# Kernel optimization log

Measured on AMD Instinct MI355X. Metric: run time of the kernel, lower is better.

## Reference

```python
import jax, jax.numpy as jnp
import numpy as np

N_NODES = 100000


def gcn_conv(x, edge_index, W, b):
    """GCNConv: out = D^-1/2 (A + I) D^-1/2 (x W) + b, with added self-loops."""
    n = x.shape[0]
    xw = x @ W  # [N, C]
    loop = jnp.arange(n, dtype=edge_index.dtype)
    src = jnp.concatenate([edge_index[0], loop])  # [E+N]
    dst = jnp.concatenate([edge_index[1], loop])
    deg = jax.ops.segment_sum(jnp.ones_like(dst, dtype=xw.dtype), dst, num_segments=n)
    dinv = jax.lax.rsqrt(jnp.where(deg > 0, deg, 1.0))
    norm = dinv[src] * dinv[dst]  # [E+N]
    msgs = xw[src] * norm[:, None]  # gather + scale
    out = jax.ops.segment_sum(msgs, dst, num_segments=n)  # scatter-add
    return out + b


def setup_inputs() -> dict:
    key = jax.random.key(0)
    k1, k2, k3, k4, k5 = jax.random.split(key, 5)
    F_in, C1, C2 = 256, 64, 40
    E = 3200000
    x = jax.random.normal(k1, (N_NODES, F_in), dtype=jnp.float32)
    edge_index = jax.random.randint(k2, (2, E), 0, N_NODES, dtype=jnp.int64)
    W1 = jax.random.normal(k3, (F_in, C1), dtype=jnp.float32) / np.sqrt(F_in)
    b1 = jnp.zeros((C1,), dtype=jnp.float32)
    W2 = jax.random.normal(k4, (C1, C2), dtype=jnp.float32) / np.sqrt(C1)
    b2 = jnp.zeros((C2,), dtype=jnp.float32)
    return {"x": x, "edge_index": edge_index, "W1": W1, "b1": b1, "W2": W2, "b2": b2}


def reference(x, edge_index, W1, b1, W2, b2):
    h1 = jax.nn.relu(gcn_conv(x, edge_index, W1, b1))
    # dropout is identity in eval mode (training=False)
    h2 = gcn_conv(h1, edge_index, W2, b2)
    return jax.nn.log_softmax(h2, axis=1)
```

## Files before the change

### kernel.cpp

```cpp
#include <hip/hip_runtime.h>
#include <math.h>

#define NN 100000
#define NB 256
#define RANGE 392
#define CAP 56
#define BCAP 13824
#define NBLK_PART 512

typedef unsigned int uint;
typedef __attribute__((ext_vector_type(8))) short short8;
typedef __attribute__((ext_vector_type(4))) float f32x4;


__global__ __launch_bounds__(256) void partition_kernel(const int* __restrict__ src,
                                                        const int* __restrict__ dst,
                                                        int* __restrict__ bcur,
                                                        unsigned* __restrict__ bkt, int E) {
    __shared__ unsigned stage[NB * CAP];
    __shared__ int lcnt[NB];
    __shared__ int baseS[NB];
    for (int i = threadIdx.x; i < NB; i += 256) lcnt[i] = 0;
    __syncthreads();

    const int nq = E >> 2;
    const int stride = gridDim.x * blockDim.x;
    for (int q = blockIdx.x * blockDim.x + threadIdx.x; q < nq; q += stride) {
        const int4 s4 = ((const int4*)src)[q];
        const int4 d4 = ((const int4*)dst)[q];
#pragma unroll
        for (int k = 0; k < 4; k++) {
            const int s = (&s4.x)[k];
            const int d = (&d4.x)[k];
            const unsigned b = (unsigned)d / RANGE;
            const unsigned ent = ((unsigned)s << 9) | ((unsigned)d - b * RANGE);
            const int slot = atomicAdd(&lcnt[b], 1);
            if (slot < CAP) {
                stage[b * CAP + slot] = ent;
            } else {
                const int pos = atomicAdd(&bcur[b], 1);
                if (pos < BCAP) bkt[(size_t)b * BCAP + pos] = ent;
            }
        }
    }
    const int gid = blockIdx.x * blockDim.x + threadIdx.x;
    if (gid < (E & 3)) {
        const int e = (E & ~3) + gid;
        const int s = src[e], d = dst[e];
        const unsigned b = (unsigned)d / RANGE;
        const unsigned ent = ((unsigned)s << 9) | ((unsigned)d - b * RANGE);
        const int pos = atomicAdd(&bcur[b], 1);
        if (pos < BCAP) bkt[(size_t)b * BCAP + pos] = ent;
    }
    __syncthreads();

    if (threadIdx.x < NB) {
        const int c = min(lcnt[threadIdx.x], CAP);
        baseS[threadIdx.x] = (c > 0) ? atomicAdd(&bcur[threadIdx.x], c) : 0;
    }
    __syncthreads();

    const int w = threadIdx.x >> 6, l = threadIdx.x & 63;
    for (int b = w; b < NB; b += 4) {
        const int cnt = min(lcnt[b], CAP);
        const int base = baseS[b];
        for (int i = l; i < cnt; i += 64) {
            const int pos = base + i;
            if (pos < BCAP) bkt[(size_t)b * BCAP + pos] = stage[b * CAP + i];
        }
    }
}


__global__ __launch_bounds__(256) void bucket_sort_kernel(const int* __restrict__ bcur,
                                                          unsigned* __restrict__ bkt,
                                                          int* __restrict__ row_off,
                                                          int* __restrict__ deg,
                                                          float* __restrict__ dinv, int n) {
    __shared__ int sortedS[BCAP];
    __shared__ int cntS[RANGE];
    __shared__ int offS[RANGE];
    const int b = blockIdx.x;
    const int tid = threadIdx.x;
    unsigned* eb = bkt + (size_t)b * BCAP;
    const int m = min(bcur[b], BCAP);

    for (int i = tid; i < RANGE; i += 256) cntS[i] = 0;
    __syncthreads();
    for (int i = tid; i < m; i += 256) atomicAdd(&cntS[(int)(eb[i] & 511u)], 1);
    __syncthreads();

    if (tid < 64) {
        const int l = tid;
        int carry = 0;
        for (int base = 0; base < RANGE; base += 64) {
            const int i = base + l;
            const int c = (i < RANGE) ? cntS[i] : 0;
            int v = c;
#pragma unroll
            for (int off = 1; off < 64; off <<= 1) {
                const int t2 = __shfl_up(v, off);
                if (l >= off) v += t2;
            }
            if (i < RANGE) offS[i] = carry + v - c;
            carry += __shfl(v, 63);
        }
    }
    __syncthreads();

    for (int i = tid; i < RANGE; i += 256) {
        const int node = b * RANGE + i;
        if (node < n) {
            row_off[node] = b * BCAP + offS[i];
            deg[node] = cntS[i];
            dinv[node] = rsqrtf((float)cntS[i] + 1.0f);
        }
    }
    __syncthreads();

    for (int i = tid; i < m; i += 256) {
        const unsigned e = eb[i];
        const int pos = atomicAdd(&offS[(int)(e & 511u)], 1);
        sortedS[pos] = (int)(e >> 9);
    }
    __syncthreads();

    for (int i = tid; i < m; i += 256) eb[i] = (unsigned)sortedS[i];
}

__device__ inline uint pack_bf16(float a, float b) {
    uint ua = __float_as_uint(a), ub = __float_as_uint(b);
    ua = (ua + 0x7fffu + ((ua >> 16) & 1u)) >> 16;
    ub = (ub + 0x7fffu + ((ub >> 16) & 1u)) & 0xffff0000u;
    return ua | ub;
}
__device__ inline unsigned short bf16r(float f) {
    uint u = __float_as_uint(f);
    return (unsigned short)((u + 0x7fffu + ((u >> 16) & 1u)) >> 16);
}
__device__ inline void acc_bf16x8(float* acc, uint4 v) {
    const uint u[4] = {v.x, v.y, v.z, v.w};
#pragma unroll
    for (int i = 0; i < 4; i++) {
        acc[2 * i]     += __uint_as_float(u[i] << 16);
        acc[2 * i + 1] += __uint_as_float(u[i] & 0xffff0000u);
    }
}


template <int K, int CREAL>
__global__ __launch_bounds__(256) void gemm_mfma_kernel(const float* __restrict__ x,
                                                        const float* __restrict__ W,
                                                        const float* __restrict__ dinv,
                                                        unsigned short* __restrict__ y,
                                                        int n) {
    constexpr int KP = K + 8;
    __shared__ unsigned short wt[64 * KP];
    __shared__ unsigned short as[128 * 40];
    const int t = threadIdx.x;
    const int l = t & 63;
    const int w = t >> 6;
    const int lane15 = l & 15;
    const int quad = l >> 4;
    const int row0 = blockIdx.x * 128;

    if (blockIdx.x == 0 && t < CREAL) y[(size_t)n * CREAL + t] = 0;

    for (int idx = t; idx < K * 16; idx += 256) {
        const int k = idx >> 4;
        const int c4 = (idx & 15) * 4;
        float4 g = make_float4(0.f, 0.f, 0.f, 0.f);
        if (c4 < CREAL) g = *(const float4*)(W + (size_t)k * CREAL + c4);
        wt[(c4 + 0) * KP + k] = bf16r(g.x);
        wt[(c4 + 1) * KP + k] = bf16r(g.y);
        wt[(c4 + 2) * KP + k] = bf16r(g.z);
        wt[(c4 + 3) * KP + k] = bf16r(g.w);
    }

    f32x4 acc[2][4];
#pragma unroll
    for (int mt = 0; mt < 2; mt++)
#pragma unroll
        for (int nt = 0; nt < 4; nt++) acc[mt][nt] = (f32x4){0.f, 0.f, 0.f, 0.f};

    float4 g[4];
#pragma unroll
    for (int p = 0; p < 4; p++) {
        const int idx = t + p * 256;
        const int row = idx >> 3;
        const int kq = idx & 7;
        const int gr = min(row0 + row, n - 1);
        g[p] = *(const float4*)(x + (size_t)gr * K + kq * 4);
    }

    for (int kc = 0; kc < K; kc += 32) {
        __syncthreads();
#pragma unroll
        for (int p = 0; p < 4; p++) {
            const int idx = t + p * 256;
            const int row = idx >> 3;
            const int kq = idx & 7;
            uint2 pk;
            pk.x = pack_bf16(g[p].x, g[p].y);
            pk.y = pack_bf16(g[p].z, g[p].w);
            *(uint2*)(as + row * 40 + kq * 4) = pk;
        }
        if (kc + 32 < K) {
#pragma unroll
            for (int p = 0; p < 4; p++) {
                const int idx = t + p * 256;
                const int row = idx >> 3;
                const int kq = idx & 7;
                const int gr = min(row0 + row, n - 1);
                g[p] = *(const float4*)(x + (size_t)gr * K + kc + 32 + kq * 4);
            }
        }
        __syncthreads();

        short8 bf[4];
#pragma unroll
        for (int nt = 0; nt < 4; nt++)
            bf[nt] = *(const short8*)(wt + (nt * 16 + lane15) * KP + kc + quad * 8);
#pragma unroll
        for (int mt = 0; mt < 2; mt++) {
            const short8 af =
                *(const short8*)(as + (w * 32 + mt * 16 + lane15) * 40 + quad * 8);
#pragma unroll
            for (int nt = 0; nt < 4; nt++)
                acc[mt][nt] =
                    __builtin_amdgcn_mfma_f32_16x16x32_bf16(af, bf[nt], acc[mt][nt], 0, 0, 0);
        }
    }

#pragma unroll
    for (int mt = 0; mt < 2; mt++) {
#pragma unroll
        for (int r = 0; r < 4; r++) {
            const int row = row0 + w * 32 + mt * 16 + quad * 4 + r;
            if (row < n) {
                const float di = dinv[row];
#pragma unroll
                for (int nt = 0; nt < 4; nt++) {
                    const int col = nt * 16 + lane15;
                    if (col < CREAL)
                        y[(size_t)row * CREAL + col] = bf16r(acc[mt][nt][r] * di);
                }
            }
        }
    }
}


__global__ __launch_bounds__(256) void agg64_kernel(const unsigned short* __restrict__ y,
                                                    const int* __restrict__ row_off,
                                                    const int* __restrict__ deg,
                                                    const unsigned* __restrict__ nbr,
                                                    const float* __restrict__ dinv,
                                                    const float* __restrict__ b,
                                                    float* __restrict__ out, int n) {
    int node = blockIdx.x * 4 + (threadIdx.x >> 6);
    if (node >= n) return;
    const int l = threadIdx.x & 63;
    const int g = l >> 3;
    const int cq = l & 7;

    const int start = row_off[node];
    const int dg = deg[node];

    float acc[8];
#pragma unroll
    for (int i = 0; i < 8; i++) acc[i] = 0.f;

    for (int base = 0; base < dg; base += 64) {
        const int m = min(64, dg - base);
        const int idx = (l < m) ? (int)nbr[start + base + l] : n;
        for (int j0 = 0; j0 < m; j0 += 16) {
            const int sA = __shfl(idx, j0 + g);
            const int sB = __shfl(idx, j0 + 8 + g);
            const uint4 vA = ((const uint4*)(y + (size_t)sA * 64))[cq];
            const uint4 vB = ((const uint4*)(y + (size_t)sB * 64))[cq];
            acc_bf16x8(acc, vA);
            acc_bf16x8(acc, vB);
        }
    }
#pragma unroll
    for (int off = 8; off < 64; off <<= 1)
#pragma unroll
        for (int i = 0; i < 8; i++) acc[i] += __shfl_xor(acc[i], off);

    float self[8];
#pragma unroll
    for (int i = 0; i < 8; i++) self[i] = 0.f;
    acc_bf16x8(self, ((const uint4*)(y + (size_t)node * 64))[cq]);
    const float di = dinv[node];
    const float4 bv0 = *(const float4*)(b + cq * 8);
    const float4 bv1 = *(const float4*)(b + cq * 8 + 4);
    const float bb[8] = {bv0.x, bv0.y, bv0.z, bv0.w, bv1.x, bv1.y, bv1.z, bv1.w};
    if (l < 8) {
        float4 o0, o1;
        o0.x = fmaxf((acc[0] + self[0]) * di + bb[0], 0.f);
        o0.y = fmaxf((acc[1] + self[1]) * di + bb[1], 0.f);
        o0.z = fmaxf((acc[2] + self[2]) * di + bb[2], 0.f);
        o0.w = fmaxf((acc[3] + self[3]) * di + bb[3], 0.f);
        o1.x = fmaxf((acc[4] + self[4]) * di + bb[4], 0.f);
        o1.y = fmaxf((acc[5] + self[5]) * di + bb[5], 0.f);
        o1.z = fmaxf((acc[6] + self[6]) * di + bb[6], 0.f);
        o1.w = fmaxf((acc[7] + self[7]) * di + bb[7], 0.f);
        *(float4*)(out + (size_t)node * 64 + l * 8) = o0;
        *(float4*)(out + (size_t)node * 64 + l * 8 + 4) = o1;
    }
}


__global__ __launch_bounds__(256) void agg40_lsm_kernel(const unsigned short* __restrict__ y,
                                                        const int* __restrict__ row_off,
                                                        const int* __restrict__ deg,
                                                        const unsigned* __restrict__ nbr,
                                                        const float* __restrict__ dinv,
                                                        const float* __restrict__ b,
                                                        float* __restrict__ out, int n) {
    int node = blockIdx.x * 4 + (threadIdx.x >> 6);
    if (node >= n) return;
    const int l = threadIdx.x & 63;
    const int cq0 = l / 12;
    const int g = l - cq0 * 12;
    const int cq = min(cq0, 4);
    const bool lead = (g == 0) && (cq0 < 5);

    const int start = row_off[node];
    const int dg = deg[node];

    float acc[8];
#pragma unroll
    for (int i = 0; i < 8; i++) acc[i] = 0.f;

    for (int base = 0; base < dg; base += 60) {
        const int m = min(60, dg - base);
        const int idx = (l < m) ? (int)nbr[start + base + l] : n;
        for (int r = 0; r * 12 < m; ++r) {
            const int s = __shfl(idx, r * 12 + g);
            const uint4 v = *((const uint4*)(y + (size_t)s * 40) + cq);
            acc_bf16x8(acc, v);
        }
    }

#pragma unroll
    for (int i = 0; i < 8; i++) { const float t = __shfl_down(acc[i], 8); if (g < 4) acc[i] += t; }
#pragma unroll
    for (int i = 0; i < 8; i++) { const float t = __shfl_down(acc[i], 4); if (g < 4) acc[i] += t; }
#pragma unroll
    for (int i = 0; i < 8; i++) { const float t = __shfl_down(acc[i], 2); if (g < 2) acc[i] += t; }
#pragma unroll
    for (int i = 0; i < 8; i++) { const float t = __shfl_down(acc[i], 1); if (g == 0) acc[i] += t; }

    if (lead) {
        const uint4 v = *((const uint4*)(y + (size_t)node * 40) + cq);
        acc_bf16x8(acc, v);
    }

    const float di = dinv[node];
    const float4 bv0 = *(const float4*)(b + cq * 8);
    const float4 bv1 = *(const float4*)(b + cq * 8 + 4);
    const float bb[8] = {bv0.x, bv0.y, bv0.z, bv0.w, bv1.x, bv1.y, bv1.z, bv1.w};
    float h[8];
#pragma unroll
    for (int i = 0; i < 8; i++) h[i] = acc[i] * di + bb[i];

    float mx = -INFINITY;
#pragma unroll
    for (int i = 0; i < 8; i++) mx = fmaxf(mx, h[i]);
    {
        const float m0 = __shfl(mx, 0), m1 = __shfl(mx, 12), m2 = __shfl(mx, 24),
                    m3 = __shfl(mx, 36), m4 = __shfl(mx, 48);
        mx = fmaxf(fmaxf(fmaxf(m0, m1), fmaxf(m2, m3)), m4);
    }
    float es = 0.f;
#pragma unroll
    for (int i = 0; i < 8; i++) es += __expf(h[i] - mx);
    {
        const float e0 = __shfl(es, 0), e1 = __shfl(es, 12), e2 = __shfl(es, 24),
                    e3 = __shfl(es, 36), e4 = __shfl(es, 48);
        es = ((e0 + e1) + (e2 + e3)) + e4;
    }
    const float ls = mx + __logf(es);

    if (lead) {
        float4 o0, o1;
        o0.x = h[0] - ls; o0.y = h[1] - ls; o0.z = h[2] - ls; o0.w = h[3] - ls;
        o1.x = h[4] - ls; o1.y = h[5] - ls; o1.z = h[6] - ls; o1.w = h[7] - ls;
        *(float4*)(out + (size_t)node * 40 + cq * 8) = o0;
        *(float4*)(out + (size_t)node * 40 + cq * 8 + 4) = o1;
    }
}


extern "C" void kernel_launch(void* const* d_in, const int* in_sizes, int n_in,
                              void* d_out, int out_size, void* d_ws, size_t ws_size,
                              hipStream_t stream) {
    const float* x  = (const float*)d_in[0];
    const int* edges = (const int*)d_in[1];
    const float* W1 = (const float*)d_in[2];
    const float* b1 = (const float*)d_in[3];
    const float* W2 = (const float*)d_in[4];
    const float* b2 = (const float*)d_in[5];
    float* out = (float*)d_out;

    const int n = NN;
    const int E = in_sizes[1] / 2;

    char* ws = (char*)d_ws;
    size_t off = 0;
    auto alloc = [&](size_t bytes) -> void* {
        void* p = ws + off;
        off += (bytes + 255) & ~(size_t)255;
        return p;
    };
    int*            bcur    = (int*)alloc((size_t)NB * 4);
    unsigned*       bkt     = (unsigned*)alloc((size_t)NB * BCAP * 4);
    int*            row_off = (int*)alloc((size_t)n * 4);
    int*            deg     = (int*)alloc((size_t)n * 4);
    float*          dinv    = (float*)alloc((size_t)n * 4);
    float*          h1      = (float*)alloc((size_t)n * 64 * 4);
    unsigned short* y1      = (unsigned short*)alloc((size_t)(n + 1) * 64 * 2);
    unsigned short* y2      = y1;

    const int* src = edges;
    const int* dst = edges + E;

    hipMemsetAsync(bcur, 0, (size_t)NB * 4, stream);
    partition_kernel<<<NBLK_PART, 256, 0, stream>>>(src, dst, bcur, bkt, E);
    bucket_sort_kernel<<<NB, 256, 0, stream>>>(bcur, bkt, row_off, deg, dinv, n);

    const int gblk = (n + 127) / 128;

    gemm_mfma_kernel<256, 64><<<gblk, 256, 0, stream>>>(x, W1, dinv, y1, n);
    agg64_kernel<<<(n + 3) / 4, 256, 0, stream>>>(y1, row_off, deg, bkt, dinv, b1, h1, n);

    gemm_mfma_kernel<64, 40><<<gblk, 256, 0, stream>>>(h1, W2, dinv, y2, n);
    agg40_lsm_kernel<<<(n + 3) / 4, 256, 0, stream>>>(y2, row_off, deg, bkt, dinv, b2, out, n);
}
```

Baseline: 371.1 us.

## Pad layer-2 features to 64-wide rows, remap lanes, use packed f32x2 accumulation

The GEMM now always writes 64-column bf16 rows, so the 40-channel layer's gathered rows are 128-byte aligned. The layer-2 aggregation lanes are remapped so that five consecutive lanes cover one neighbor row, making each neighbor read a contiguous 80-byte span. The reduction tree is rewritten to match the new mapping. Accumulators use two-wide float vectors so the compiler can emit packed FP32 adds. In exchange, layer-2 intermediate storage grows and unused padded columns are written.

```diff
diff --git a/kernel.cpp b/kernel.cpp
--- a/kernel.cpp
+++ b/kernel.cpp
@@ -11,6 +11,7 @@
 typedef unsigned int uint;
 typedef __attribute__((ext_vector_type(8))) short short8;
 typedef __attribute__((ext_vector_type(4))) float f32x4;
+typedef __attribute__((ext_vector_type(2))) float f32x2;
 
 
 __global__ __launch_bounds__(256) void partition_kernel(const int* __restrict__ src,
@@ -138,12 +139,14 @@
     uint u = __float_as_uint(f);
     return (unsigned short)((u + 0x7fffu + ((u >> 16) & 1u)) >> 16);
 }
-__device__ inline void acc_bf16x8(float* acc, uint4 v) {
+__device__ inline void acc_bf16x8p(f32x2* acc, uint4 v) {
     const uint u[4] = {v.x, v.y, v.z, v.w};
 #pragma unroll
     for (int i = 0; i < 4; i++) {
-        acc[2 * i]     += __uint_as_float(u[i] << 16);
-        acc[2 * i + 1] += __uint_as_float(u[i] & 0xffff0000u);
+        f32x2 t;
+        t.x = __uint_as_float(u[i] << 16);
+        t.y = __uint_as_float(u[i] & 0xffff0000u);
+        acc[i] += t;
     }
 }
 
@@ -164,7 +167,7 @@
     const int quad = l >> 4;
     const int row0 = blockIdx.x * 128;
 
-    if (blockIdx.x == 0 && t < CREAL) y[(size_t)n * CREAL + t] = 0;
+    if (blockIdx.x == 0 && t < 64) y[(size_t)n * 64 + t] = 0;
 
     for (int idx = t; idx < K * 16; idx += 256) {
         const int k = idx >> 4;
@@ -240,11 +243,8 @@
             if (row < n) {
                 const float di = dinv[row];
 #pragma unroll
-                for (int nt = 0; nt < 4; nt++) {
-                    const int col = nt * 16 + lane15;
-                    if (col < CREAL)
-                        y[(size_t)row * CREAL + col] = bf16r(acc[mt][nt][r] * di);
-                }
+                for (int nt = 0; nt < 4; nt++)
+                    y[(size_t)row * 64 + nt * 16 + lane15] = bf16r(acc[mt][nt][r] * di);
             }
         }
     }
@@ -267,9 +267,9 @@
     const int start = row_off[node];
     const int dg = deg[node];
 
-    float acc[8];
-#pragma unroll
-    for (int i = 0; i < 8; i++) acc[i] = 0.f;
+    f32x2 acc[4];
+#pragma unroll
+    for (int i = 0; i < 4; i++) acc[i] = (f32x2){0.f, 0.f};
 
     for (int base = 0; base < dg; base += 64) {
         const int m = min(64, dg - base);
@@ -279,33 +279,35 @@
             const int sB = __shfl(idx, j0 + 8 + g);
             const uint4 vA = ((const uint4*)(y + (size_t)sA * 64))[cq];
             const uint4 vB = ((const uint4*)(y + (size_t)sB * 64))[cq];
-            acc_bf16x8(acc, vA);
-            acc_bf16x8(acc, vB);
-        }
-    }
+            acc_bf16x8p(acc, vA);
+            acc_bf16x8p(acc, vB);
+        }
+    }
+    float* af = (float*)acc;
 #pragma unroll
     for (int off = 8; off < 64; off <<= 1)
 #pragma unroll
-        for (int i = 0; i < 8; i++) acc[i] += __shfl_xor(acc[i], off);
-
-    float self[8];
-#pragma unroll
-    for (int i = 0; i < 8; i++) self[i] = 0.f;
-    acc_bf16x8(self, ((const uint4*)(y + (size_t)node * 64))[cq]);
+        for (int i = 0; i < 8; i++) af[i] += __shfl_xor(af[i], off);
+
+    f32x2 self[4];
+#pragma unroll
+    for (int i = 0; i < 4; i++) self[i] = (f32x2){0.f, 0.f};
+    acc_bf16x8p(self, ((const uint4*)(y + (size_t)node * 64))[cq]);
+    const float* sf = (const float*)self;
     const float di = dinv[node];
     const float4 bv0 = *(const float4*)(b + cq * 8);
     const float4 bv1 = *(const float4*)(b + cq * 8 + 4);
     const float bb[8] = {bv0.x, bv0.y, bv0.z, bv0.w, bv1.x, bv1.y, bv1.z, bv1.w};
     if (l < 8) {
         float4 o0, o1;
-        o0.x = fmaxf((acc[0] + self[0]) * di + bb[0], 0.f);
-        o0.y = fmaxf((acc[1] + self[1]) * di + bb[1], 0.f);
-        o0.z = fmaxf((acc[2] + self[2]) * di + bb[2], 0.f);
-        o0.w = fmaxf((acc[3] + self[3]) * di + bb[3], 0.f);
-        o1.x = fmaxf((acc[4] + self[4]) * di + bb[4], 0.f);
-        o1.y = fmaxf((acc[5] + self[5]) * di + bb[5], 0.f);
-        o1.z = fmaxf((acc[6] + self[6]) * di + bb[6], 0.f);
-        o1.w = fmaxf((acc[7] + self[7]) * di + bb[7], 0.f);
+        o0.x = fmaxf((af[0] + sf[0]) * di + bb[0], 0.f);
+        o0.y = fmaxf((af[1] + sf[1]) * di + bb[1], 0.f);
+        o0.z = fmaxf((af[2] + sf[2]) * di + bb[2], 0.f);
+        o0.w = fmaxf((af[3] + sf[3]) * di + bb[3], 0.f);
+        o1.x = fmaxf((af[4] + sf[4]) * di + bb[4], 0.f);
+        o1.y = fmaxf((af[5] + sf[5]) * di + bb[5], 0.f);
+        o1.z = fmaxf((af[6] + sf[6]) * di + bb[6], 0.f);
+        o1.w = fmaxf((af[7] + sf[7]) * di + bb[7], 0.f);
         *(float4*)(out + (size_t)node * 64 + l * 8) = o0;
         *(float4*)(out + (size_t)node * 64 + l * 8 + 4) = o1;
     }
@@ -322,40 +324,40 @@
     int node = blockIdx.x * 4 + (threadIdx.x >> 6);
     if (node >= n) return;
     const int l = threadIdx.x & 63;
-    const int cq0 = l / 12;
-    const int g = l - cq0 * 12;
-    const int cq = min(cq0, 4);
-    const bool lead = (g == 0) && (cq0 < 5);
+    int gg = l / 5;
+    int cq = l - gg * 5;
+    if (l >= 60) { gg = 11; cq = l - 60; }
 
     const int start = row_off[node];
     const int dg = deg[node];
 
-    float acc[8];
-#pragma unroll
-    for (int i = 0; i < 8; i++) acc[i] = 0.f;
+    f32x2 acc[4];
+#pragma unroll
+    for (int i = 0; i < 4; i++) acc[i] = (f32x2){0.f, 0.f};
 
     for (int base = 0; base < dg; base += 60) {
         const int m = min(60, dg - base);
         const int idx = (l < m) ? (int)nbr[start + base + l] : n;
         for (int r = 0; r * 12 < m; ++r) {
-            const int s = __shfl(idx, r * 12 + g);
-            const uint4 v = *((const uint4*)(y + (size_t)s * 40) + cq);
-            acc_bf16x8(acc, v);
-        }
-    }
-
-#pragma unroll
-    for (int i = 0; i < 8; i++) { const float t = __shfl_down(acc[i], 8); if (g < 4) acc[i] += t; }
-#pragma unroll
-    for (int i = 0; i < 8; i++) { const float t = __shfl_down(acc[i], 4); if (g < 4) acc[i] += t; }
-#pragma unroll
-    for (int i = 0; i < 8; i++) { const float t = __shfl_down(acc[i], 2); if (g < 2) acc[i] += t; }
-#pragma unroll
-    for (int i = 0; i < 8; i++) { const float t = __shfl_down(acc[i], 1); if (g == 0) acc[i] += t; }
-
-    if (lead) {
-        const uint4 v = *((const uint4*)(y + (size_t)node * 40) + cq);
-        acc_bf16x8(acc, v);
+            const int s = __shfl(idx, r * 12 + gg);
+            const uint4 v = *((const uint4*)(y + (size_t)s * 64) + cq);
+            acc_bf16x8p(acc, v);
+        }
+    }
+
+    float* af = (float*)acc;
+#pragma unroll
+    for (int i = 0; i < 8; i++) { const float t = __shfl_down(af[i], 30); if (l < 30) af[i] += t; }
+#pragma unroll
+    for (int i = 0; i < 8; i++) { const float t = __shfl_down(af[i], 15); if (l < 15) af[i] += t; }
+#pragma unroll
+    for (int i = 0; i < 8; i++) { const float t = __shfl_down(af[i], 5);  if (l < 5)  af[i] += t; }
+#pragma unroll
+    for (int i = 0; i < 8; i++) { const float t = __shfl_down(af[i], 10); if (l < 5)  af[i] += t; }
+
+    if (l < 5) {
+        const uint4 v = *((const uint4*)(y + (size_t)node * 64) + cq);
+        acc_bf16x8p(acc, v);
     }
 
     const float di = dinv[node];
@@ -364,27 +366,27 @@
     const float bb[8] = {bv0.x, bv0.y, bv0.z, bv0.w, bv1.x, bv1.y, bv1.z, bv1.w};
     float h[8];
 #pragma unroll
-    for (int i = 0; i < 8; i++) h[i] = acc[i] * di + bb[i];
+    for (int i = 0; i < 8; i++) h[i] = af[i] * di + bb[i];
 
     float mx = -INFINITY;
 #pragma unroll
     for (int i = 0; i < 8; i++) mx = fmaxf(mx, h[i]);
     {
-        const float m0 = __shfl(mx, 0), m1 = __shfl(mx, 12), m2 = __shfl(mx, 24),
-                    m3 = __shfl(mx, 36), m4 = __shfl(mx, 48);
+        const float m0 = __shfl(mx, 0), m1 = __shfl(mx, 1), m2 = __shfl(mx, 2),
+                    m3 = __shfl(mx, 3), m4 = __shfl(mx, 4);
         mx = fmaxf(fmaxf(fmaxf(m0, m1), fmaxf(m2, m3)), m4);
     }
     float es = 0.f;
 #pragma unroll
     for (int i = 0; i < 8; i++) es += __expf(h[i] - mx);
     {
-        const float e0 = __shfl(es, 0), e1 = __shfl(es, 12), e2 = __shfl(es, 24),
-                    e3 = __shfl(es, 36), e4 = __shfl(es, 48);
+        const float e0 = __shfl(es, 0), e1 = __shfl(es, 1), e2 = __shfl(es, 2),
+                    e3 = __shfl(es, 3), e4 = __shfl(es, 4);
         es = ((e0 + e1) + (e2 + e3)) + e4;
     }
     const float ls = mx + __logf(es);
 
-    if (lead) {
+    if (l < 5) {
         float4 o0, o1;
         o0.x = h[0] - ls; o0.y = h[1] - ls; o0.z = h[2] - ls; o0.w = h[3] - ls;
         o1.x = h[4] - ls; o1.y = h[5] - ls; o1.z = h[6] - ls; o1.w = h[7] - ls;
```

Measured after the change: 370.9 us. Within noise of the previous version (-0.1%).
